# Kernel optimization log

Hardware: AMD Instinct MI355X
Metric: run time of the kernel (lower is better)

## Reference

```python
import jax, jax.numpy as jnp
import numpy as np

ORDER = 2            # spline order kx = ky
H = W = 7            # control_grid_dims
KSZ = 3.0            # kernel_size -> bbox = (-1.5, 1.5)
OUT, IN = 32, 32     # out_channels, in_groups (groups=1)
N = 32768            # number of query points
BBOX = KSZ / 2.0


def _make_knots(n_coef, lo, hi, order):
    # clamped knot vector of length n_coef + order + 1 (as scipy produces)
    n_interior = n_coef - order - 1
    interior = np.linspace(lo, hi, n_interior + 2)[1:-1]
    t = np.concatenate([[lo] * (order + 1), interior, [hi] * (order + 1)])
    return jnp.asarray(t, dtype=jnp.float32)


def setup_inputs() -> dict:
    key = jax.random.key(0)
    k1, k2 = jax.random.split(key)
    # query points strictly inside the bbox
    xy = jax.random.uniform(k1, (N, 2), dtype=jnp.float32,
                            minval=-BBOX * 0.95, maxval=BBOX * 0.95)
    # control coefficients C: [out_channels, in_groups, h, w]
    C = jax.random.normal(k2, (OUT, IN, H, W), dtype=jnp.float32) * 0.1
    Tx = _make_knots(H, -BBOX, BBOX, ORDER)
    Ty = _make_knots(W, -BBOX, BBOX, ORDER)
    return {"xy": xy, "Tx": Tx, "Ty": Ty, "C": C}


def _find_span(T, v, p):
    # torch: (T <= v).min(dim=-1) -> first False index, minus 1; if all True -> len(T)-p-2
    ss = jnp.searchsorted(T, v, side="right")          # number of knots <= v
    return jnp.where(ss == T.shape[0], T.shape[0] - p - 2, ss - 1)


def _safe_div(num, den):
    return num / jnp.where(den == 0, jnp.ones_like(den), den)


def reference(xy, Tx, Ty, C):
    px = py = ORDER
    X = xy[:, 0]
    Y = xy[:, 1]
    kx = _find_span(Tx, X, px)   # [N] knot spans
    ky = _find_span(Ty, Y, py)

    dim = OUT * IN
    Ctrl = C.reshape(dim, H, W)
    offs = jnp.arange(px + 1)
    ix = kx[:, None] - px + offs                 # [N, px+1]
    iy = ky[:, None] - py + offs                 # [N, py+1]
    # gather local (px+1)x(py+1) control patch per point: [N, Dim, px+1, py+1]
    D = Ctrl[:, ix[:, :, None], iy[:, None, :]]
    D = jnp.transpose(D, (1, 0, 2, 3))

    rng = jnp.arange(px)
    # de Boor recursion along x
    for r in range(1, px + 1):
        t_lo = Tx[kx[:, None] - px + 1 + rng]    # [N, px]
        t_hi = Tx[kx[:, None] + 2 - r + rng]
        alphax = _safe_div(X[:, None] - t_lo, t_hi - t_lo)
        for j in range(px, r - 1, -1):
            a = alphax[:, j - 1][:, None, None]
            D = D.at[:, :, j, :].set((1 - a) * D[:, :, j - 1, :] + a * D[:, :, j, :])
    # de Boor recursion along y (on the collapsed x row px)
    for r in range(1, py + 1):
        t_lo = Ty[ky[:, None] - py + 1 + rng]
        t_hi = Ty[ky[:, None] + 2 - r + rng]
        alphay = _safe_div(Y[:, None] - t_lo, t_hi - t_lo)
        for j in range(py, r - 1, -1):
            a = alphay[:, j - 1][:, None]
            D = D.at[:, :, px, j].set((1 - a) * D[:, :, px, j - 1] + a * D[:, :, px, j])

    return D[:, :, px, py].reshape(xy.shape[0], OUT, IN)
```

## Files before the change

### kernel.cpp

```cpp
#include <hip/hip_runtime.h>


#define NPTS   32768
#define DIM    1024
#define MT     (NPTS / 16)
#define WELEM  (MT * 2 * 64 * 8)

typedef _Float16 f16x8 __attribute__((ext_vector_type(8)));
typedef float    f32x4 __attribute__((ext_vector_type(4)));

__device__ __forceinline__ float safe_div(float n, float d) {
    return (d == 0.0f) ? n : (n / d);
}

__device__ __forceinline__ void span_weights(float v, const float* __restrict__ T,
                                             int& k, float& w0, float& w1, float& w2) {
    float t3 = T[3], t4 = T[4], t5 = T[5], t6 = T[6];
    k = 2 + (v >= t3) + (v >= t4) + (v >= t5) + (v >= t6);
    float Tm1 = T[k - 1], T0 = T[k], Tp1 = T[k + 1], Tp2 = T[k + 2];
    float a10 = safe_div(v - Tm1, Tp1 - Tm1);
    float a11 = safe_div(v - T0,  Tp2 - T0);
    float a21 = safe_div(v - T0,  Tp1 - T0);
    w0 = (1.0f - a21) * (1.0f - a10);
    w1 = (1.0f - a21) * a10 + a21 * (1.0f - a11);
    w2 = a21 * a11;
}

__global__ __launch_bounds__(256) void prep_kernel(
    const float* __restrict__ xy,
    const float* __restrict__ Tx,
    const float* __restrict__ Ty,
    const float* __restrict__ C,
    _Float16* __restrict__ Wp,
    _Float16* __restrict__ Cp)
{
    const int b = blockIdx.x;
    const int t = threadIdx.x;
    if (b < MT / 2) {
        const int id   = b * 256 + t;
        const int lane = id & 63;
        const int step = (id >> 6) & 1;
        const int tile = id >> 7;
        const int n    = tile * 16 + (lane & 15);
        const int g    = lane >> 4;

        const float2 pt = ((const float2*)xy)[n];
        int kx, ky;
        float wx0, wx1, wx2, wy0, wy1, wy2;
        span_weights(pt.x, Tx, kx, wx0, wx1, wx2);
        span_weights(pt.y, Ty, ky, wy0, wy1, wy2);
        const int off = (kx - 2) * 7 + (ky - 2);

        f16x8 frag;
#pragma unroll
        for (int j = 0; j < 8; ++j) {
            const int k   = step * 32 + g * 8 + j;
            const int rel = k - off;
            const float va = (rel >= 14) ? wx2 : ((rel >= 7) ? wx1 : wx0);
            const int   bb = rel - ((rel >= 14) ? 14 : ((rel >= 7) ? 7 : 0));
            const float vb = (bb == 0) ? wy0 : ((bb == 1) ? wy1 : wy2);
            const bool valid = (rel >= 0) && (rel <= 16) && (bb >= 0) && (bb <= 2);
            frag[j] = (_Float16)(valid ? va * vb : 0.0f);
        }
        *(f16x8*)(Wp + (size_t)id * 8) = frag;
    } else if (b < MT / 2 + 32) {
        const int id    = (b - MT / 2) * 256 + t;
        const int lane  = id & 63;
        const int step  = (id >> 6) & 1;
        const int ctile = id >> 7;
        const int ch    = ctile * 16 + (lane & 15);
        const int g     = lane >> 4;

        f16x8 frag;
#pragma unroll
        for (int j = 0; j < 8; ++j) {
            const int k = step * 32 + g * 8 + j;
            frag[j] = (_Float16)((k < 49) ? C[(size_t)ch * 49 + k] : 0.0f);
        }
        *(f16x8*)(Cp + (size_t)id * 8) = frag;
    }
}

__global__ __launch_bounds__(256, 4) void spline_mfma_kernel(
    const _Float16* __restrict__ Wp,
    const _Float16* __restrict__ Cp,
    float* __restrict__ out)
{
    __shared__ _Float16 wlds[8 * 2 * 64 * 8];
    __shared__ float    tbuf[4][1024];

    const int t    = threadIdx.x;
    const int lane = t & 63;
    const int w    = t >> 6;

    const int bid    = blockIdx.x;
    const int swz    = ((bid & 7) << 7) | (bid >> 3);
    const int chgrp  = swz & 3;
    const int pchunk = swz >> 2;

    {
        const f16x8* src = (const f16x8*)(Wp + (size_t)pchunk * (8 * 2 * 64 * 8));
        f16x8* dst = (f16x8*)wlds;
#pragma unroll
        for (int i = 0; i < 4; ++i)
            dst[t + i * 256] = src[t + i * 256];
    }

    f16x8 af[4][2];
#pragma unroll
    for (int ct = 0; ct < 4; ++ct)
#pragma unroll
        for (int st = 0; st < 2; ++st) {
            const int ctg = chgrp * 16 + w * 4 + ct;
            af[ct][st] = *(const f16x8*)(Cp + ((size_t)(ctg * 2 + st) * 64 + lane) * 8);
        }

    __syncthreads();

    const int p  = lane & 15;
    const int h  = lane >> 4;
    const int cb = lane & 15;
    float* const wbuf = &tbuf[w][0];

#pragma unroll
    for (int pt = 0; pt < 8; ++pt) {
        const int ptile = pchunk * 8 + pt;

        const f16x8 b0 = *(const f16x8*)&wlds[((pt * 2 + 0) * 64 + lane) * 8];
        const f16x8 b1 = *(const f16x8*)&wlds[((pt * 2 + 1) * 64 + lane) * 8];

        f32x4 acc[4];
#pragma unroll
        for (int ct = 0; ct < 4; ++ct) {
            f32x4 z; z[0] = 0.0f; z[1] = 0.0f; z[2] = 0.0f; z[3] = 0.0f;
            acc[ct] = __builtin_amdgcn_mfma_f32_16x16x32_f16(af[ct][0], b0, z, 0, 0, 0);
        }
#pragma unroll
        for (int ct = 0; ct < 4; ++ct)
            acc[ct] = __builtin_amdgcn_mfma_f32_16x16x32_f16(af[ct][1], b1, acc[ct], 0, 0, 0);

#pragma unroll
        for (int ct = 0; ct < 4; ++ct) {
            const int g16 = ct * 4 + h;
            const int col = (g16 & 8) | ((g16 ^ p) & 7);
            *(f32x4*)(wbuf + p * 64 + (col << 2)) = acc[ct];
        }

#pragma unroll
        for (int gg = 0; gg < 4; ++gg) {
            const int pr  = gg * 4 + h;
            const int col = (cb & 8) | ((cb ^ pr) & 7);
            f32x4 v = *(const f32x4*)(wbuf + pr * 64 + (col << 2));
            float* dst = out + (size_t)(ptile * 16 + pr) * DIM
                             + chgrp * 256 + w * 64 + cb * 4;
            __builtin_nontemporal_store(v, (f32x4*)dst);
        }
    }
}

extern "C" void kernel_launch(void* const* d_in, const int* in_sizes, int n_in,
                              void* d_out, int out_size, void* d_ws, size_t ws_size,
                              hipStream_t stream) {
    const float* xy = (const float*)d_in[0];
    const float* Tx = (const float*)d_in[1];
    const float* Ty = (const float*)d_in[2];
    const float* C  = (const float*)d_in[3];
    float* out = (float*)d_out;

    _Float16* Wp = (_Float16*)d_ws;
    _Float16* Cp = Wp + WELEM;

    prep_kernel<<<MT / 2 + 32, 256, 0, stream>>>(xy, Tx, Ty, C, Wp, Cp);
    spline_mfma_kernel<<<4 * (MT / 8), 256, 0, stream>>>(Wp, Cp, out);
}
```

Before: 34.66 us.

## Fuse per-point spline weight generation into the MFMA kernel

```diff
diff --git a/kernel.cpp b/kernel.cpp
--- a/kernel.cpp
+++ b/kernel.cpp
@@ -4,7 +4,6 @@
 #define NPTS   32768
 #define DIM    1024
 #define MT     (NPTS / 16)
-#define WELEM  (MT * 2 * 64 * 8)
 
 typedef _Float16 f16x8 __attribute__((ext_vector_type(8)));
 typedef float    f32x4 __attribute__((ext_vector_type(4)));
@@ -26,63 +25,30 @@
     w2 = a21 * a11;
 }
 
-__global__ __launch_bounds__(256) void prep_kernel(
+__global__ __launch_bounds__(256) void prep_cp_kernel(
+    const float* __restrict__ C,
+    _Float16* __restrict__ Cp)
+{
+    const int id    = blockIdx.x * 256 + threadIdx.x;
+    const int lane  = id & 63;
+    const int step  = (id >> 6) & 1;
+    const int ctile = id >> 7;
+    const int ch    = ctile * 16 + (lane & 15);
+    const int g     = lane >> 4;
+
+    f16x8 frag;
+#pragma unroll
+    for (int j = 0; j < 8; ++j) {
+        const int k = step * 32 + g * 8 + j;
+        frag[j] = (_Float16)((k < 49) ? C[(size_t)ch * 49 + k] : 0.0f);
+    }
+    *(f16x8*)(Cp + (size_t)id * 8) = frag;
+}
+
+__global__ __launch_bounds__(256, 4) void spline_mfma_kernel(
     const float* __restrict__ xy,
     const float* __restrict__ Tx,
     const float* __restrict__ Ty,
-    const float* __restrict__ C,
-    _Float16* __restrict__ Wp,
-    _Float16* __restrict__ Cp)
-{
-    const int b = blockIdx.x;
-    const int t = threadIdx.x;
-    if (b < MT / 2) {
-        const int id   = b * 256 + t;
-        const int lane = id & 63;
-        const int step = (id >> 6) & 1;
-        const int tile = id >> 7;
-        const int n    = tile * 16 + (lane & 15);
-        const int g    = lane >> 4;
-
-        const float2 pt = ((const float2*)xy)[n];
-        int kx, ky;
-        float wx0, wx1, wx2, wy0, wy1, wy2;
-        span_weights(pt.x, Tx, kx, wx0, wx1, wx2);
-        span_weights(pt.y, Ty, ky, wy0, wy1, wy2);
-        const int off = (kx - 2) * 7 + (ky - 2);
-
-        f16x8 frag;
-#pragma unroll
-        for (int j = 0; j < 8; ++j) {
-            const int k   = step * 32 + g * 8 + j;
-            const int rel = k - off;
-            const float va = (rel >= 14) ? wx2 : ((rel >= 7) ? wx1 : wx0);
-            const int   bb = rel - ((rel >= 14) ? 14 : ((rel >= 7) ? 7 : 0));
-            const float vb = (bb == 0) ? wy0 : ((bb == 1) ? wy1 : wy2);
-            const bool valid = (rel >= 0) && (rel <= 16) && (bb >= 0) && (bb <= 2);
-            frag[j] = (_Float16)(valid ? va * vb : 0.0f);
-        }
-        *(f16x8*)(Wp + (size_t)id * 8) = frag;
-    } else if (b < MT / 2 + 32) {
-        const int id    = (b - MT / 2) * 256 + t;
-        const int lane  = id & 63;
-        const int step  = (id >> 6) & 1;
-        const int ctile = id >> 7;
-        const int ch    = ctile * 16 + (lane & 15);
-        const int g     = lane >> 4;
-
-        f16x8 frag;
-#pragma unroll
-        for (int j = 0; j < 8; ++j) {
-            const int k = step * 32 + g * 8 + j;
-            frag[j] = (_Float16)((k < 49) ? C[(size_t)ch * 49 + k] : 0.0f);
-        }
-        *(f16x8*)(Cp + (size_t)id * 8) = frag;
-    }
-}
-
-__global__ __launch_bounds__(256, 4) void spline_mfma_kernel(
-    const _Float16* __restrict__ Wp,
     const _Float16* __restrict__ Cp,
     float* __restrict__ out)
 {
@@ -98,12 +64,32 @@
     const int chgrp  = swz & 3;
     const int pchunk = swz >> 2;
 
-    {
-        const f16x8* src = (const f16x8*)(Wp + (size_t)pchunk * (8 * 2 * 64 * 8));
-        f16x8* dst = (f16x8*)wlds;
+    if (t < 128) {
+        const int tl   = t >> 4;
+        const int prow = t & 15;
+        const float2 pt2 = ((const float2*)xy)[pchunk * 128 + t];
+        int kx, ky;
+        float wx0, wx1, wx2, wy0, wy1, wy2;
+        span_weights(pt2.x, Tx, kx, wx0, wx1, wx2);
+        span_weights(pt2.y, Ty, ky, wy0, wy1, wy2);
+        const int off = (kx - 2) * 7 + (ky - 2);
 #pragma unroll
-        for (int i = 0; i < 4; ++i)
-            dst[t + i * 256] = src[t + i * 256];
+        for (int st = 0; st < 2; ++st)
+#pragma unroll
+            for (int g = 0; g < 4; ++g) {
+                f16x8 frag;
+#pragma unroll
+                for (int j = 0; j < 8; ++j) {
+                    const int k   = st * 32 + g * 8 + j;
+                    const int rel = k - off;
+                    const float va = (rel >= 14) ? wx2 : ((rel >= 7) ? wx1 : wx0);
+                    const int   bb = rel - ((rel >= 14) ? 14 : ((rel >= 7) ? 7 : 0));
+                    const float vb = (bb == 0) ? wy0 : ((bb == 1) ? wy1 : wy2);
+                    const bool valid = (rel >= 0) && (rel <= 16) && (bb >= 0) && (bb <= 2);
+                    frag[j] = (_Float16)(valid ? va * vb : 0.0f);
+                }
+                *(f16x8*)&wlds[(size_t)((tl * 2 + st) * 64 + g * 16 + prow) * 8] = frag;
+            }
     }
 
     f16x8 af[4][2];
@@ -126,8 +112,8 @@
     for (int pt = 0; pt < 8; ++pt) {
         const int ptile = pchunk * 8 + pt;
 
-        const f16x8 b0 = *(const f16x8*)&wlds[((pt * 2 + 0) * 64 + lane) * 8];
-        const f16x8 b1 = *(const f16x8*)&wlds[((pt * 2 + 1) * 64 + lane) * 8];
+        const f16x8 b0 = *(const f16x8*)&wlds[(size_t)((pt * 2 + 0) * 64 + lane) * 8];
+        const f16x8 b1 = *(const f16x8*)&wlds[(size_t)((pt * 2 + 1) * 64 + lane) * 8];
 
         f32x4 acc[4];
 #pragma unroll
@@ -167,9 +153,8 @@
     const float* C  = (const float*)d_in[3];
     float* out = (float*)d_out;
 
-    _Float16* Wp = (_Float16*)d_ws;
-    _Float16* Cp = Wp + WELEM;
+    _Float16* Cp = (_Float16*)d_ws;
 
-    prep_kernel<<<MT / 2 + 32, 256, 0, stream>>>(xy, Tx, Ty, C, Wp, Cp);
-    spline_mfma_kernel<<<4 * (MT / 8), 256, 0, stream>>>(Wp, Cp, out);
+    prep_cp_kernel<<<32, 256, 0, stream>>>(C, Cp);
+    spline_mfma_kernel<<<4 * (MT / 8), 256, 0, stream>>>(xy, Tx, Ty, Cp, out);
 }
```

Measured after the change: 35.57 us. 1.03x slower.
